# Optimization experiments

Measured on AMD Instinct MI355X. Metric: run time of the kernel, lower is better.

## Reference

```python
import jax, jax.numpy as jnp
import numpy as np

B, T, D, H, HORIZON, OUT = 1024, 64, 128, 128, 24, 1
ATT = 64  # attention MLP hidden size


def _p(key, shape, scale=0.05):
    return scale * jax.random.normal(key, shape, dtype=jnp.float32)


def setup_inputs() -> dict:
    ks = jax.random.split(jax.random.key(0), 20)
    return dict(
        X=jax.random.normal(ks[0], (B, T, D), jnp.float32),
        y_hist=jax.random.normal(ks[1], (B, T), jnp.float32),
        We_w=_p(ks[2], (ATT, 2 * H + 1)), We_b=_p(ks[3], (ATT,)),
        ve_w=_p(ks[4], (1, ATT)), ve_b=_p(ks[5], (1,)),
        enc_Wih=_p(ks[6], (4 * H, D)), enc_Whh=_p(ks[7], (4 * H, H)),
        enc_bih=_p(ks[8], (4 * H,)), enc_bhh=_p(ks[9], (4 * H,)),
        dec_Wih=_p(ks[10], (4 * H, 1)), dec_Whh=_p(ks[11], (4 * H, H)),
        dec_bih=_p(ks[12], (4 * H,)), dec_bhh=_p(ks[13], (4 * H,)),
        Wd_w=_p(ks[14], (ATT, 3 * H)), Wd_b=_p(ks[15], (ATT,)),
        vd_w=_p(ks[16], (1, ATT)), vd_b=_p(ks[17], (1,)),
        fc_w=_p(ks[18], (OUT, 2 * H + T)), fc_b=_p(ks[19], (OUT,)),
    )


def _lstm_cell(x, h, c, Wih, Whh, bih, bhh):
    # torch.nn.LSTMCell gate order: i, f, g, o
    gates = x @ Wih.T + bih + h @ Whh.T + bhh
    i, f, g, o = jnp.split(gates, 4, axis=1)
    c2 = jax.nn.sigmoid(f) * c + jax.nn.sigmoid(i) * jnp.tanh(g)
    h2 = jax.nn.sigmoid(o) * jnp.tanh(c2)
    return h2, c2


def _forward(X, y_hist, We_w, We_b, ve_w, ve_b,
             enc_Wih, enc_Whh, enc_bih, enc_bhh,
             dec_Wih, dec_Whh, dec_bih, dec_bhh,
             Wd_w, Wd_b, vd_w, vd_b, fc_w, fc_b):
    batch = X.shape[0]
    # --- encoder with input attention (vectorized over the per-k python loop) ---
    W_hs = We_w[:, :2 * H]       # weights on [h_prev, s_prev]
    w_feat = We_w[:, 2 * H]      # weight on the scalar feature, shape (ATT,)

    def enc_step(carry, x_t):
        h, c = carry
        base = jnp.concatenate([h, c], axis=1) @ W_hs.T + We_b        # (B, ATT)
        energy = jnp.tanh(base[:, None, :] + x_t[:, :, None] * w_feat)  # (B, D, ATT)
        scores = energy @ ve_w[0] + ve_b[0]                            # (B, D)
        alpha = jax.nn.softmax(scores, axis=1)
        x_tilde = alpha * x_t
        h2, c2 = _lstm_cell(x_tilde, h, c, enc_Wih, enc_Whh, enc_bih, enc_bhh)
        return (h2, c2), h2

    h0 = jnp.zeros((batch, H), X.dtype)
    c0 = jnp.zeros((batch, H), X.dtype)
    _, enc_h = jax.lax.scan(enc_step, (h0, c0), X.transpose(1, 0, 2))
    enc_hiddens = enc_h.transpose(1, 0, 2)  # (B, T, H)

    # --- decoder with temporal attention ---
    # Wd_w columns ordered as cat([encoder_hiddens, d_prev, c_prev])
    enc_proj = jnp.einsum('bth,kh->btk', enc_hiddens, Wd_w[:, :H])  # (B, T, ATT)
    Wd_d, Wd_c = Wd_w[:, H:2 * H], Wd_w[:, 2 * H:]

    def dec_step(carry, _):
        d, cc, y_prev = carry
        dc = d @ Wd_d.T + cc @ Wd_c.T + Wd_b                # (B, ATT)
        energy = jnp.tanh(enc_proj + dc[:, None, :])         # (B, T, ATT)
        score = energy @ vd_w[0] + vd_b[0]                   # (B, T)
        beta = jax.nn.softmax(score, axis=1)
        context = jnp.einsum('bt,bth->bh', beta, enc_hiddens)  # (B, H)
        d2, cc2 = _lstm_cell(y_prev, d, cc, dec_Wih, dec_Whh, dec_bih, dec_bhh)
        fc_in = jnp.concatenate([d2, context, y_hist], axis=1)  # (B, 2H+T)
        out = fc_in @ fc_w.T + fc_b                              # (B, 1)
        return (d2, cc2, out), out

    d0 = jnp.zeros((batch, H), X.dtype)
    cd0 = jnp.zeros((batch, H), X.dtype)
    y0 = y_hist[:, -1:]
    _, outs = jax.lax.scan(dec_step, (d0, cd0, y0), None, length=HORIZON)
    return outs.transpose(1, 0, 2)  # (B, horizon, output_dim)


def reference(X, y_hist, We_w, We_b, ve_w, ve_b,
              enc_Wih, enc_Whh, enc_bih, enc_bhh,
              dec_Wih, dec_Whh, dec_bih, dec_bhh,
              Wd_w, Wd_b, vd_w, vd_b, fc_w, fc_b):
    return _forward(X, y_hist, We_w, We_b, ve_w, ve_b,
                    enc_Wih, enc_Whh, enc_bih, enc_bhh,
                    dec_Wih, dec_Whh, dec_bih, dec_bhh,
                    Wd_w, Wd_b, vd_w, vd_b, fc_w, fc_b)
```

## Files before the change

### kernel.cpp

```cpp
#include <hip/hip_runtime.h>
#include <hip/hip_bf16.h>


#define B_    1024
#define T_    64
#define D_    128
#define H_    128
#define HOR_  24
#define ATT_  64
#define BB    4
#define LOG2E 1.4426950408889634f
#define C127  (1.f/127.f)
#define KLAG  8.245856315e-05f

typedef float f32x4  __attribute__((ext_vector_type(4)));
typedef short bf16x8 __attribute__((ext_vector_type(8)));
typedef int   i32x4  __attribute__((ext_vector_type(4)));

#define MFMA16(a,b,c) __builtin_amdgcn_mfma_f32_16x16x32_bf16((a),(b),(c),0,0,0)
#define MFMAI8(a,b,c) __builtin_amdgcn_mfma_i32_16x16x64_i8((a),(b),(c),0,0,0)

#define WHS_E    0
#define WDDC_E   16384
#define WDENC_E  32768
#define WENC8_B  81920
#define WDEC8_B  212992
#define SENC_B   278528
#define SDEC_B   280576

__device__ __forceinline__ short f2b(float f) {
  union { float f; unsigned u; } c; c.f = f;
  unsigned r = c.u + 0x7fffu + ((c.u >> 16) & 1u);
  return (short)(r >> 16);
}
__device__ __forceinline__ float b2f(short s) {
  union { unsigned u; float f; } c; c.u = ((unsigned)(unsigned short)s) << 16;
  return c.f;
}
__device__ __forceinline__ float fexp2(float x) { return __builtin_amdgcn_exp2f(x); }
__device__ __forceinline__ float frcp (float x) { return __builtin_amdgcn_rcpf(x); }
__device__ __forceinline__ float tanh_acc(float x) {
  float e = fexp2(x * 2.885390081777927f);
  return 1.f - 2.f * frcp(1.f + e);
}
__device__ __forceinline__ float sigm(float x) {
  return frcp(1.f + fexp2(-LOG2E * x));
}

template<int CTRL>
__device__ __forceinline__ float dppmov(float v) {
  return __builtin_bit_cast(float,
      __builtin_amdgcn_mov_dpp(__builtin_bit_cast(int, v), CTRL, 0xF, 0xF, true));
}
__device__ __forceinline__ float swz16(float v) {
  return __builtin_bit_cast(float,
      __builtin_amdgcn_ds_swizzle(__builtin_bit_cast(int, v), 0x401F));
}
__device__ __forceinline__ float wsum64(float v) {
  v += dppmov<0xB1>(v);
  v += dppmov<0x4E>(v);
  v += dppmov<0x141>(v);
  v += dppmov<0x140>(v);
  v += swz16(v);
  v += __shfl_xor(v, 32, 64);
  return v;
}
__device__ __forceinline__ float wmax64(float v) {
  v = fmaxf(v, dppmov<0xB1>(v));
  v = fmaxf(v, dppmov<0x4E>(v));
  v = fmaxf(v, dppmov<0x141>(v));
  v = fmaxf(v, dppmov<0x140>(v));
  v = fmaxf(v, swz16(v));
  v = fmaxf(v, __shfl_xor(v, 32, 64));
  return v;
}
__device__ __forceinline__ float gsum8(float v) {
  v += dppmov<0xB1>(v);
  v += dppmov<0x4E>(v);
  v += dppmov<0x141>(v);
  return v;
}

__global__ void prep_bf(const float* __restrict__ We_w,
                        const float* __restrict__ Wd_w,
                        char* __restrict__ ws8) {
  int e = blockIdx.x * 256 + threadIdx.x;
  if (e >= 40960) return;
  short* f16 = (short*)ws8;
  int region = e >> 14;
  int er = e & 16383;
  int fi = er >> 9, li = (er >> 3) & 63, jq = er & 7;
  int kt = fi >> 2, nt = fi & 3;
  int k = kt * 32 + ((li >> 4) << 3) + jq, n = nt * 16 + (li & 15);
  float v;
  if (region == 0)      v = We_w[n * 257 + k];
  else if (region == 1) v = (k < 128) ? Wd_w[n * 384 + 128 + k]
                                      : Wd_w[n * 384 + 256 + (k - 128)];
  else                  v = Wd_w[n * 384 + k];
  f16[e] = f2b(v);
}

__global__ void prep_q(const float* __restrict__ enc_Wih,
                       const float* __restrict__ enc_Whh,
                       const float* __restrict__ dec_Whh,
                       char* __restrict__ ws8) {
  int gw = (blockIdx.x * 256 + threadIdx.x) >> 6;
  int lane = threadIdx.x & 63;
  if (gw < 512) {
    int n = gw;
    float v[4]; float m = 0.f;
#pragma unroll
    for (int q = 0; q < 4; ++q) {
      int k = lane * 4 + q;
      v[q] = (k < 128) ? enc_Wih[n * 128 + k] : enc_Whh[n * 128 + (k - 128)];
      m = fmaxf(m, fabsf(v[q]));
    }
    m = wmax64(m);
    if (lane == 0) ((float*)(ws8 + SENC_B))[n] = m * C127;
    float inv = m > 0.f ? 127.f / m : 0.f;
    char* dst = ws8 + WENC8_B;
#pragma unroll
    for (int q = 0; q < 4; ++q) {
      int k = lane * 4 + q;
      int kt = k >> 6, grp = (k >> 4) & 3, b = k & 15, l16 = (n & 15) | (grp << 4);
      dst[((kt * 32 + (n >> 4)) * 64 + l16) * 16 + b] = (char)(int)rintf(v[q] * inv);
    }
  } else if (gw < 1024) {
    int n = gw - 512;
    float v[2]; float m = 0.f;
#pragma unroll
    for (int q = 0; q < 2; ++q) {
      int k = lane * 2 + q;
      v[q] = dec_Whh[n * 128 + k];
      m = fmaxf(m, fabsf(v[q]));
    }
    m = wmax64(m);
    if (lane == 0) ((float*)(ws8 + SDEC_B))[n] = m * C127;
    float inv = m > 0.f ? 127.f / m : 0.f;
    char* dst = ws8 + WDEC8_B;
#pragma unroll
    for (int q = 0; q < 2; ++q) {
      int k = lane * 2 + q;
      int kt = k >> 6, grp = (k >> 4) & 3, b = k & 15, l16 = (n & 15) | (grp << 4);
      dst[((kt * 32 + (n >> 4)) * 64 + l16) * 16 + b] = (char)(int)rintf(v[q] * inv);
    }
  }
}

__global__ __launch_bounds__(512, 2)
void da_rnn(const float* __restrict__ X, const float* __restrict__ y_hist,
            const float* __restrict__ We_w, const float* __restrict__ We_b,
            const float* __restrict__ ve_w,
            const float* __restrict__ enc_bih, const float* __restrict__ enc_bhh,
            const float* __restrict__ dec_Wih,
            const float* __restrict__ dec_bih, const float* __restrict__ dec_bhh,
            const float* __restrict__ Wd_b, const float* __restrict__ vd_w,
            const float* __restrict__ fc_w, const float* __restrict__ fc_b,
            const char* __restrict__ ws8, float* __restrict__ out) {
  const short* f16  = (const short*)ws8;
  const i32x4* enc8 = (const i32x4*)(ws8 + WENC8_B);
  const i32x4* dec8 = (const i32x4*)(ws8 + WDEC8_B);
  const float* senc = (const float*)(ws8 + SENC_B);
  const float* sdec = (const float*)(ws8 + SDEC_B);

  __shared__ __align__(16) char  s_A8[16][272];
  __shared__ __align__(16) short s_Ahc[16][264];
  __shared__ short s_projT[4][64][65];
  __shared__ short s_encht[4][128][66];
  __shared__ __align__(16) float s_gates[4][528];
  __shared__ __align__(16) float s_base[4][72];
  __shared__ float s_beta[4][64];
  __shared__ float s_xr[4];
  __shared__ float2 s_wv[64];
  __shared__ __align__(16) float s_web[64];
  __shared__ float s_vd[64];
  __shared__ __align__(16) float s_wdb[64];
  __shared__ float s_se[512], s_sd[512];
  __shared__ float s_encb[512], s_decb[512], s_dwih[512];
  __shared__ float s_fcw[320];

  const int tid  = threadIdx.x;
  const int lane = tid & 63;
  const int w    = tid >> 6;
  const int b0   = blockIdx.x * BB;

  if (tid < 64) {
    s_wv[tid]  = make_float2(We_w[tid * 257 + 256], ve_w[tid]);
    s_web[tid] = We_b[tid];
    s_vd[tid]  = vd_w[tid];
    s_wdb[tid] = Wd_b[tid];
  }
  if (tid < 320) s_fcw[tid] = fc_w[tid];
  s_se[tid]   = senc[tid];
  s_sd[tid]   = sdec[tid];
  s_encb[tid] = enc_bih[tid] + enc_bhh[tid];
  s_decb[tid] = dec_bih[tid] + dec_bhh[tid];
  s_dwih[tid] = dec_Wih[tid];
  for (int i = tid; i < (16 * 272) / 4; i += 512) ((int*)s_A8)[i] = 0;
  for (int i = tid; i < (16 * 264) / 2; i += 512) ((int*)s_Ahc)[i] = 0;
  if (tid < 256) s_base[tid >> 6][tid & 63] = We_b[tid & 63];

  i32x4 wg[4][4];
#pragma unroll
  for (int kt = 0; kt < 4; ++kt)
#pragma unroll
    for (int i = 0; i < 4; ++i)
      wg[kt][i] = enc8[(kt * 32 + (w + 8 * i)) * 64 + lane];
  bf16x8 wb[8], wp[4];
  if (w < 4) {
#pragma unroll
    for (int kt = 0; kt < 8; ++kt)
      wb[kt] = *(const bf16x8*)(f16 + WHS_E + ((kt * 4 + w) * 64 + lane) * 8);
  } else {
#pragma unroll
    for (int kt = 0; kt < 4; ++kt)
      wp[kt] = *(const bf16x8*)(f16 + WDENC_E + ((kt * 4 + (w - 4)) * 64 + lane) * 8);
  }

  float xf0 = 0.f, xf1 = 0.f, xi = 0.f;
  const float* Xr = X + (size_t)(b0 + (w & 3)) * T_ * D_;
  if (w < 4) {
    xf0 = Xr[lane]; xf1 = Xr[64 + lane];
    xi = 6.f * cosf((2 * (lane >> 3) + 1) * 0.19634954084936207f);
  }
  float cstE = 0.f;
  const int rE = w & 3;
  const int fE = ((w >> 2) << 6) + lane;
  i32x4 ahp[4];
#pragma unroll
  for (int i = 0; i < 4; ++i) ahp[i] = (i32x4){0, 0, 0, 0};
  __syncthreads();

  float seE[4], ebE[4];
#pragma unroll
  for (int g = 0; g < 4; ++g) {
    seE[g] = s_se[fE + 128 * g];
    ebE[g] = s_encb[fE + 128 * g];
  }
  f32x4 webq = {0.f, 0.f, 0.f, 0.f};
  if (w < 4) webq = *(const f32x4*)&s_web[(w << 4) + ((lane >> 4) << 2)];

  for (int t = 0; t < T_; ++t) {
    float x0, x1;
    if (w < 4) {
      x0 = xf0; x1 = xf1;
      const int kc = lane & 7;
      float p = 0.f;
      const float4* wvp = (const float4*)&s_wv[kc * 8];
      const float4* bp  = (const float4*)&s_base[w][kc * 8];
      float4 bA = bp[0], bB = bp[1];
#pragma unroll
      for (int q = 0; q < 4; ++q) {
        float4 wv = wvp[q];
        float bb0 = (q < 2) ? ((q & 1) ? bA.z : bA.x) : ((q & 1) ? bB.z : bB.x);
        float bb1 = (q < 2) ? ((q & 1) ? bA.w : bA.y) : ((q & 1) ? bB.w : bB.y);
        p += wv.y * tanh_acc(fmaf(xi, wv.x, bb0));
        p += wv.w * tanh_acc(fmaf(xi, wv.z, bb1));
      }
      p = gsum8(p);
      float f0 = __shfl(p,  0, 64), f1 = __shfl(p,  8, 64);
      float f2 = __shfl(p, 16, 64), f3 = __shfl(p, 24, 64);
      float f4 = __shfl(p, 32, 64), f5 = __shfl(p, 40, 64);
      float f6 = __shfl(p, 48, 64), f7 = __shfl(p, 56, 64);
      float e0, e1;
      {
        const float xb[8] = { 5.884711682f, 4.988817674f, 3.333421398f, 1.170541932f,
                             -1.170541932f, -3.333421398f, -4.988817674f, -5.884711682f};
        const float wbar[8] = { 0.1950903220f, -0.5555702330f, 0.8314696123f, -0.9807852804f,
                                0.9807852804f, -0.8314696123f, 0.5555702330f, -0.1950903220f};
        float fw[8] = {f0 * wbar[0], f1 * wbar[1], f2 * wbar[2], f3 * wbar[3],
                       f4 * wbar[4], f5 * wbar[5], f6 * wbar[6], f7 * wbar[7]};
        float u0 = fminf(fmaxf(x0, -6.f), 6.f), u1 = fminf(fmaxf(x1, -6.f), 6.f);
        float d0[8], d1[8], P0[8], P1[8];
        float pre0 = 1.f, pre1 = 1.f;
#pragma unroll
        for (int i = 0; i < 8; ++i) {
          d0[i] = u0 - xb[i]; d1[i] = u1 - xb[i];
          P0[i] = pre0;       P1[i] = pre1;
          pre0 *= d0[i];      pre1 *= d1[i];
        }
        float suf0 = 1.f, suf1 = 1.f, acc0 = 0.f, acc1 = 0.f;
#pragma unroll
        for (int i = 7; i >= 0; --i) {
          acc0 = fmaf(fw[i] * P0[i], suf0, acc0);
          acc1 = fmaf(fw[i] * P1[i], suf1, acc1);
          suf0 *= d0[i];
          suf1 *= d1[i];
        }
        e0 = fexp2(acc0 * KLAG);
        e1 = fexp2(acc1 * KLAG);
      }
      float sum = wsum64(e0 + e1);
      float mx  = wmax64(fmaxf(e0 * fabsf(x0), e1 * fabsf(x1)));
      float inv = mx > 0.f ? 127.f * frcp(mx) : 0.f;
      s_A8[w][lane]      = (char)(int)rintf(x0 * e0 * inv);
      s_A8[w][64 + lane] = (char)(int)rintf(x1 * e1 * inv);
      if (lane == 0) s_xr[w] = mx * frcp(127.f * sum);
    }
    __syncthreads();
    {
      i32x4 a0 = *(const i32x4*)&s_A8[lane & 15][  0 + ((lane >> 4) << 4)];
      i32x4 a1 = *(const i32x4*)&s_A8[lane & 15][ 64 + ((lane >> 4) << 4)];
      i32x4 ax[4];
#pragma unroll
      for (int i = 0; i < 4; ++i) {
        i32x4 z = {0, 0, 0, 0};
        ax[i] = MFMAI8(wg[1][i], a1, MFMAI8(wg[0][i], a0, z));
      }
      float sx = s_xr[lane & 3];
      if ((lane & 15) < 4) {
        int cb = (lane >> 4) << 2;
#pragma unroll
        for (int i = 0; i < 4; ++i) {
          f32x4 v;
#pragma unroll
          for (int r = 0; r < 4; ++r)
            v[r] = fmaf(sx, (float)ax[i][r], C127 * (float)ahp[i][r]);
          *(f32x4*)&s_gates[lane & 15][(w + 8 * i) * 16 + cb] = v;
        }
      }
    }
    __syncthreads();
    {
      float g_i = fmaf(s_gates[rE][fE]      , seE[0], ebE[0]);
      float g_f = fmaf(s_gates[rE][fE + 128], seE[1], ebE[1]);
      float g_g = fmaf(s_gates[rE][fE + 256], seE[2], ebE[2]);
      float g_o = fmaf(s_gates[rE][fE + 384], seE[3], ebE[3]);
      cstE = sigm(g_f) * cstE + sigm(g_i) * tanh_acc(g_g);
      float h = sigm(g_o) * tanh_acc(cstE);
      s_Ahc[rE][fE]        = f2b(h);
      s_Ahc[rE][128 + fE]  = f2b(cstE);
      s_A8[rE][128 + fE]   = (char)(int)rintf(h * 127.f);
      s_encht[rE][fE][t]   = f2b(h);
    }
    __syncthreads();
    {
      i32x4 pa2 = *(const i32x4*)&s_A8[lane & 15][128 + ((lane >> 4) << 4)];
      i32x4 pa3 = *(const i32x4*)&s_A8[lane & 15][192 + ((lane >> 4) << 4)];
#pragma unroll
      for (int i = 0; i < 4; ++i) {
        i32x4 z = {0, 0, 0, 0};
        ahp[i] = MFMAI8(wg[3][i], pa3, MFMAI8(wg[2][i], pa2, z));
      }
    }
    if (w < 4) {
      if (t < T_ - 1) {
        xf0 = Xr[(t + 1) * D_ + lane];
        xf1 = Xr[(t + 1) * D_ + 64 + lane];
      }
      f32x4 acc = {0.f, 0.f, 0.f, 0.f}, acc2 = {0.f, 0.f, 0.f, 0.f};
#pragma unroll
      for (int kt = 0; kt < 4; ++kt) {
        bf16x8 a = *(const bf16x8*)&s_Ahc[lane & 15][kt * 32 + ((lane >> 4) << 3)];
        acc = MFMA16(wb[kt], a, acc);
      }
#pragma unroll
      for (int kt = 4; kt < 8; ++kt) {
        bf16x8 a = *(const bf16x8*)&s_Ahc[lane & 15][kt * 32 + ((lane >> 4) << 3)];
        acc2 = MFMA16(wb[kt], a, acc2);
      }
      if ((lane & 15) < 4) {
        f32x4 v = acc + acc2 + webq;
        *(f32x4*)&s_base[lane & 15][(w << 4) + ((lane >> 4) << 2)] = v;
      }
    } else {
      f32x4 acc = {0.f, 0.f, 0.f, 0.f};
#pragma unroll
      for (int kt = 0; kt < 4; ++kt) {
        bf16x8 a = *(const bf16x8*)&s_Ahc[lane & 15][kt * 32 + ((lane >> 4) << 3)];
        acc = MFMA16(a, wp[kt], acc);
      }
      if (lane < 16) {
        int katt = (w - 4) * 16 + lane;
#pragma unroll
        for (int r = 0; r < 4; ++r) s_projT[r][katt][t] = f2b(acc[r]);
      }
    }
    __syncthreads();
  }

  {
    int r = tid >> 7, j = tid & 127;
    s_Ahc[r][j] = 0; s_Ahc[r][128 + j] = 0; s_A8[r][j] = 0;
  }
  i32x4 wdg[2][8];
  bf16x8 wdc[8];
  float yp = 0.f, yhd = 0.f;
  float sdC_p[8], db_p[8], dw_p[8];
  f32x4 wdbq = {0.f, 0.f, 0.f, 0.f};
  if (w >= 4) {
#pragma unroll
    for (int kt = 0; kt < 2; ++kt)
#pragma unroll
      for (int i = 0; i < 8; ++i)
        wdg[kt][i] = dec8[(kt * 32 + ((w - 4) * 8 + i)) * 64 + lane];
  } else {
#pragma unroll
    for (int kt = 0; kt < 8; ++kt)
      wdc[kt] = *(const bf16x8*)(f16 + WDDC_E + ((kt * 4 + w) * 64 + lane) * 8);
#pragma unroll
    for (int j = 0; j < 8; ++j) {
      sdC_p[j] = s_sd[lane + 64 * j] * C127;
      db_p[j]  = s_decb[lane + 64 * j];
      dw_p[j]  = s_dwih[lane + 64 * j];
    }
    wdbq = *(const f32x4*)&s_wdb[(w << 4) + ((lane >> 4) << 2)];
    yp = y_hist[(b0 + w) * T_ + (T_ - 1)];
    float pp = s_fcw[256 + lane] * y_hist[(b0 + w) * T_ + lane];
    yhd = wsum64(pp) + fc_b[0];
  }
  float dd0 = 0.f, dc0 = 0.f, dd1 = 0.f, dc1 = 0.f;
  __syncthreads();

  for (int hs = 0; hs < HOR_; ++hs) {
    if (w >= 4) {
      i32x4 a0 = *(const i32x4*)&s_A8[lane & 15][ 0 + ((lane >> 4) << 4)];
      i32x4 a1 = *(const i32x4*)&s_A8[lane & 15][64 + ((lane >> 4) << 4)];
#pragma unroll
      for (int i = 0; i < 8; ++i) {
        i32x4 z = {0, 0, 0, 0};
        i32x4 ac = MFMAI8(wdg[1][i], a1, MFMAI8(wdg[0][i], a0, z));
        if ((lane & 15) < 4) {
          f32x4 v = {(float)ac[0], (float)ac[1], (float)ac[2], (float)ac[3]};
          *(f32x4*)&s_gates[lane & 15][(((w - 4) * 8 + i) << 4) + ((lane >> 4) << 2)] = v;
        }
      }
    } else {
      if (hs > 0) {
        float cx0a = 0.f, cx0b = 0.f, cx1a = 0.f, cx1b = 0.f;
        const short* e0p = &s_encht[w][lane][0];
        const short* e1p = &s_encht[w][lane + 64][0];
#pragma unroll 8
        for (int tp = 0; tp < 32; ++tp) {
          float2 bta = *(const float2*)&s_beta[w][2 * tp];
          short2 h0v = *(const short2*)&e0p[2 * tp];
          short2 h1v = *(const short2*)&e1p[2 * tp];
          cx0a = fmaf(bta.x, b2f(h0v.x), cx0a); cx0b = fmaf(bta.y, b2f(h0v.y), cx0b);
          cx1a = fmaf(bta.x, b2f(h1v.x), cx1a); cx1b = fmaf(bta.y, b2f(h1v.y), cx1b);
        }
        float cx0 = cx0a + cx0b, cx1 = cx1a + cx1b;
        float pf = s_fcw[lane] * dd0 + s_fcw[64 + lane] * dd1
                 + s_fcw[128 + lane] * cx0 + s_fcw[192 + lane] * cx1;
        pf = wsum64(pf);
        float o = pf + yhd;
        if (lane == 0) out[(b0 + w) * HOR_ + (hs - 1)] = o;
        yp = o;
      }
      f32x4 acc = {0.f, 0.f, 0.f, 0.f}, acc2 = {0.f, 0.f, 0.f, 0.f};
#pragma unroll
      for (int kt = 0; kt < 4; ++kt) {
        bf16x8 a = *(const bf16x8*)&s_Ahc[lane & 15][kt * 32 + ((lane >> 4) << 3)];
        acc = MFMA16(wdc[kt], a, acc);
      }
#pragma unroll
      for (int kt = 4; kt < 8; ++kt) {
        bf16x8 a = *(const bf16x8*)&s_Ahc[lane & 15][kt * 32 + ((lane >> 4) << 3)];
        acc2 = MFMA16(wdc[kt], a, acc2);
      }
      if ((lane & 15) < 4) {
        f32x4 v = acc + acc2 + wdbq;
        *(f32x4*)&s_base[lane & 15][(w << 4) + ((lane >> 4) << 2)] = v;
      }
    }
    __syncthreads();
    if (w < 4) {
      float gi0 = s_gates[w][lane]       * sdC_p[0] + db_p[0] + yp * dw_p[0];
      float gi1 = s_gates[w][lane + 64]  * sdC_p[1] + db_p[1] + yp * dw_p[1];
      float gf0 = s_gates[w][lane + 128] * sdC_p[2] + db_p[2] + yp * dw_p[2];
      float gf1 = s_gates[w][lane + 192] * sdC_p[3] + db_p[3] + yp * dw_p[3];
      float gg0 = s_gates[w][lane + 256] * sdC_p[4] + db_p[4] + yp * dw_p[4];
      float gg1 = s_gates[w][lane + 320] * sdC_p[5] + db_p[5] + yp * dw_p[5];
      float go0 = s_gates[w][lane + 384] * sdC_p[6] + db_p[6] + yp * dw_p[6];
      float go1 = s_gates[w][lane + 448] * sdC_p[7] + db_p[7] + yp * dw_p[7];
      dc0 = sigm(gf0) * dc0 + sigm(gi0) * tanh_acc(gg0);
      dd0 = sigm(go0) * tanh_acc(dc0);
      dc1 = sigm(gf1) * dc1 + sigm(gi1) * tanh_acc(gg1);
      dd1 = sigm(go1) * tanh_acc(dc1);
      s_Ahc[w][lane]       = f2b(dd0);
      s_Ahc[w][lane + 64]  = f2b(dd1);
      s_Ahc[w][lane + 128] = f2b(dc0);
      s_Ahc[w][lane + 192] = f2b(dc1);
      s_A8[w][lane]      = (char)(int)rintf(dd0 * 127.f);
      s_A8[w][lane + 64] = (char)(int)rintf(dd1 * 127.f);
    } else {
      const int r = w - 4;
      float sA = 0.f, sB = 0.f, sC = 0.f, sD = 0.f;
#pragma unroll 4
      for (int k = 0; k < 64; k += 4) {
        sA += s_vd[k]     * tanh_acc(b2f(s_projT[r][k][lane])     + s_base[r][k]);
        sB += s_vd[k + 1] * tanh_acc(b2f(s_projT[r][k + 1][lane]) + s_base[r][k + 1]);
        sC += s_vd[k + 2] * tanh_acc(b2f(s_projT[r][k + 2][lane]) + s_base[r][k + 2]);
        sD += s_vd[k + 3] * tanh_acc(b2f(s_projT[r][k + 3][lane]) + s_base[r][k + 3]);
      }
      float s = (sA + sB) + (sC + sD);
      float e = fexp2(s * LOG2E);
      float ssum = wsum64(e);
      s_beta[r][lane] = e * frcp(ssum);
    }
    __syncthreads();
  }
  if (w < 4) {
    float cx0a = 0.f, cx0b = 0.f, cx1a = 0.f, cx1b = 0.f;
    const short* e0p = &s_encht[w][lane][0];
    const short* e1p = &s_encht[w][lane + 64][0];
#pragma unroll 8
    for (int tp = 0; tp < 32; ++tp) {
      float2 bta = *(const float2*)&s_beta[w][2 * tp];
      short2 h0v = *(const short2*)&e0p[2 * tp];
      short2 h1v = *(const short2*)&e1p[2 * tp];
      cx0a = fmaf(bta.x, b2f(h0v.x), cx0a); cx0b = fmaf(bta.y, b2f(h0v.y), cx0b);
      cx1a = fmaf(bta.x, b2f(h1v.x), cx1a); cx1b = fmaf(bta.y, b2f(h1v.y), cx1b);
    }
    float cx0 = cx0a + cx0b, cx1 = cx1a + cx1b;
    float pf = s_fcw[lane] * dd0 + s_fcw[64 + lane] * dd1
             + s_fcw[128 + lane] * cx0 + s_fcw[192 + lane] * cx1;
    pf = wsum64(pf);
    float o = pf + yhd;
    if (lane == 0) out[(b0 + w) * HOR_ + (HOR_ - 1)] = o;
  }
}

extern "C" void kernel_launch(void* const* d_in, const int* in_sizes, int n_in,
                              void* d_out, int out_size, void* d_ws, size_t ws_size,
                              hipStream_t stream) {
  (void)in_sizes; (void)n_in; (void)out_size; (void)ws_size;
  const float* X       = (const float*)d_in[0];
  const float* y_hist  = (const float*)d_in[1];
  const float* We_w    = (const float*)d_in[2];
  const float* We_b    = (const float*)d_in[3];
  const float* ve_w    = (const float*)d_in[4];
  const float* enc_Wih = (const float*)d_in[6];
  const float* enc_Whh = (const float*)d_in[7];
  const float* enc_bih = (const float*)d_in[8];
  const float* enc_bhh = (const float*)d_in[9];
  const float* dec_Wih = (const float*)d_in[10];
  const float* dec_Whh = (const float*)d_in[11];
  const float* dec_bih = (const float*)d_in[12];
  const float* dec_bhh = (const float*)d_in[13];
  const float* Wd_w    = (const float*)d_in[14];
  const float* Wd_b    = (const float*)d_in[15];
  const float* vd_w    = (const float*)d_in[16];
  const float* fc_w    = (const float*)d_in[18];
  const float* fc_b    = (const float*)d_in[19];

  char* ws8  = (char*)d_ws;
  float* out = (float*)d_out;

  prep_bf<<<160, 256, 0, stream>>>(We_w, Wd_w, ws8);
  prep_q <<<256, 256, 0, stream>>>(enc_Wih, enc_Whh, dec_Whh, ws8);
  da_rnn <<<B_ / BB, 512, 0, stream>>>(X, y_hist, We_w, We_b, ve_w,
                                       enc_bih, enc_bhh, dec_Wih, dec_bih, dec_bhh,
                                       Wd_b, vd_w, fc_w, fc_b, ws8, out);
}
```

Measured before the change: 300.2 us.

## Remap encoder LSTM cell to per-wave gate ownership and drop a barrier

```diff
diff --git a/kernel.cpp b/kernel.cpp
--- a/kernel.cpp
+++ b/kernel.cpp
@@ -223,19 +223,20 @@
     xf0 = Xr[lane]; xf1 = Xr[64 + lane];
     xi = 6.f * cosf((2 * (lane >> 3) + 1) * 0.19634954084936207f);
   }
-  float cstE = 0.f;
-  const int rE = w & 3;
-  const int fE = ((w >> 2) << 6) + lane;
+  float cM = 0.f;
+  const int bM   = lane >> 4;
+  const int phil = lane & 15;
+  const int phig = (w << 4) + phil;
   i32x4 ahp[4];
 #pragma unroll
   for (int i = 0; i < 4; ++i) ahp[i] = (i32x4){0, 0, 0, 0};
   __syncthreads();
 
-  float seE[4], ebE[4];
-#pragma unroll
-  for (int g = 0; g < 4; ++g) {
-    seE[g] = s_se[fE + 128 * g];
-    ebE[g] = s_encb[fE + 128 * g];
+  float seM[4], ebM[4];
+#pragma unroll
+  for (int q = 0; q < 4; ++q) {
+    seM[q] = s_se[q * 128 + phig];
+    ebM[q] = s_encb[q * 128 + phig];
   }
   f32x4 webq = {0.f, 0.f, 0.f, 0.f};
   if (w < 4) webq = *(const f32x4*)&s_web[(w << 4) + ((lane >> 4) << 2)];
@@ -307,31 +308,31 @@
         i32x4 z = {0, 0, 0, 0};
         ax[i] = MFMAI8(wg[1][i], a1, MFMAI8(wg[0][i], a0, z));
       }
+      float* scr = ((float*)s_gates) + w * 264;
       float sx = s_xr[lane & 3];
       if ((lane & 15) < 4) {
-        int cb = (lane >> 4) << 2;
+        int off = ((lane & 15) << 4) + ((lane >> 4) << 2);
 #pragma unroll
         for (int i = 0; i < 4; ++i) {
           f32x4 v;
 #pragma unroll
           for (int r = 0; r < 4; ++r)
             v[r] = fmaf(sx, (float)ax[i][r], C127 * (float)ahp[i][r]);
-          *(f32x4*)&s_gates[lane & 15][(w + 8 * i) * 16 + cb] = v;
+          *(f32x4*)&scr[i * 64 + off] = v;
         }
       }
-    }
-    __syncthreads();
-    {
-      float g_i = fmaf(s_gates[rE][fE]      , seE[0], ebE[0]);
-      float g_f = fmaf(s_gates[rE][fE + 128], seE[1], ebE[1]);
-      float g_g = fmaf(s_gates[rE][fE + 256], seE[2], ebE[2]);
-      float g_o = fmaf(s_gates[rE][fE + 384], seE[3], ebE[3]);
-      cstE = sigm(g_f) * cstE + sigm(g_i) * tanh_acc(g_g);
-      float h = sigm(g_o) * tanh_acc(cstE);
-      s_Ahc[rE][fE]        = f2b(h);
-      s_Ahc[rE][128 + fE]  = f2b(cstE);
-      s_A8[rE][128 + fE]   = (char)(int)rintf(h * 127.f);
-      s_encht[rE][fE][t]   = f2b(h);
+      asm volatile("" ::: "memory");
+      int ra = (bM << 4) + phil;
+      float g_i = fmaf(scr[      ra], seM[0], ebM[0]);
+      float g_f = fmaf(scr[ 64 + ra], seM[1], ebM[1]);
+      float g_g = fmaf(scr[128 + ra], seM[2], ebM[2]);
+      float g_o = fmaf(scr[192 + ra], seM[3], ebM[3]);
+      cM = sigm(g_f) * cM + sigm(g_i) * tanh_acc(g_g);
+      float h = sigm(g_o) * tanh_acc(cM);
+      s_Ahc[bM][phig]       = f2b(h);
+      s_Ahc[bM][128 + phig] = f2b(cM);
+      s_A8[bM][128 + phig]  = (char)(int)rintf(h * 127.f);
+      s_encht[bM][phig][t]  = f2b(h);
     }
     __syncthreads();
     {
```

After: 300.7 us. About the same (+0.2%).
